# Kernel optimization log

Measured on AMD Instinct MI355X. Metric: run time of the kernel, lower is better.

The kernel has to match this reference:

```python
import jax, jax.numpy as jnp
import numpy as np

N_Q = 4; K = 4; IMG = 28; PAD = IMG + 2  # pad right/bottom so edge windows exist
N_WIN = 14 * 14  # stride-2 windows over 28x28


def _window_idx():
    # Faithful to torch: flatten the (possibly truncated) window row-major,
    # then pad with zeros AT THE END of the flattened vector.
    zero = PAD * PAD - 1  # padded image is zero there
    rows = []
    for i in range(0, IMG - 1, 2):
        for j in range(0, IMG - 1, 2):
            h = min(K, IMG - i); w = min(K, IMG - j)
            ids = [(i + r) * PAD + (j + c) for r in range(h) for c in range(w)]
            ids += [zero] * (K * K - len(ids))
            rows.append(ids)
    return np.asarray(rows, np.int32)  # [196, 16]

_WIDX = _window_idx()
# wire 0 is the most-significant bit of the 16-dim statevector index
_BITS = ((np.arange(16)[None, :] >> (3 - np.arange(4))[:, None]) & 1)
_ZSIGN = (1.0 - 2.0 * _BITS).astype(np.float32)  # [4, 16] PauliZ eigenvalues
# Four CRZ gates (control i, target (i+1)%4) are all diagonal -> combined diagonal phase
_CRZ_SIGNS = np.zeros(16, np.float32)
for _b in range(16):
    s = 0
    for _i in range(4):
        c = (_b >> (3 - _i)) & 1
        t = (_b >> (3 - ((_i + 1) % 4))) & 1
        s += c * (2 * t - 1)
    _CRZ_SIGNS[_b] = s
_H = (np.array([[1, 1], [1, -1]], np.complex64) / np.sqrt(2.0)).astype(np.complex64)


def _rz(a):  # a [B] -> [B,2,2]: diag(e^{-i a/2}, e^{+i a/2})
    em = jnp.exp(-0.5j * a); ep = jnp.exp(0.5j * a); z = jnp.zeros_like(em)
    return jnp.stack([jnp.stack([em, z], -1), jnp.stack([z, ep], -1)], -2)


def _ry(a):  # a [...] -> [...,2,2]
    c = jnp.cos(0.5 * a); s = jnp.sin(0.5 * a)
    return jnp.stack([jnp.stack([c, -s], -1), jnp.stack([s, c], -1)], -2).astype(jnp.complex64)


def _apply1q(state, U, w):  # state [B,16], U [B,2,2] or [2,2], wire w (0=MSB)
    L = 2 ** w; R = 2 ** (3 - w)
    s = state.reshape(-1, L, 2, R)
    if U.ndim == 2:
        out = jnp.einsum('ij,bajc->baic', U, s)
    else:
        out = jnp.einsum('bij,bajc->baic', U, s)
    return out.reshape(-1, 16)


def reference(x, crz_theta, ry_theta, fc1_w, fc1_b, fc2_w, fc2_b):
    B = x.shape[0]
    xp = jnp.pad(x[:, 0], ((0, 0), (0, 2), (0, 2))).reshape(B, -1)  # [B, 900]
    wins = xp[:, jnp.asarray(_WIDX)]              # [B, 196, 16]
    wins = jnp.transpose(wins, (1, 0, 2))         # [196, B, 16] for scan

    crz_diag = jnp.exp(0.5j * crz_theta * jnp.asarray(_CRZ_SIGNS))  # [16]
    Ry = _ry(ry_theta)                            # shared trainable RY, [2,2]
    H = jnp.asarray(_H)
    zsT = jnp.asarray(_ZSIGN).T                   # [16, 4]

    def step(state, f):  # state [B,16] complex64 persists ACROSS windows (no reset in source)
        for w in range(4):
            # compose H then the encoder rotations on this wire into one 2x2 per batch elem
            U = jnp.broadcast_to(H, (B, 2, 2))
            n = 5 if w < 3 else 1  # wire 3 only gets rz(f[15])
            for i in range(n):
                a = f[:, w * 5 + i]
                M = _rz(a) if i % 2 == 0 else _ry(a)  # gates = rz,ry,rz,ry,rz
                U = jnp.einsum('bij,bjk->bik', M, U)
            state = _apply1q(state, U, w)
        state = state * crz_diag[None, :]          # ring of CRZ gates (diagonal)
        for w in range(4):
            state = _apply1q(state, Ry, w)
        probs = state.real ** 2 + state.imag ** 2
        return state, probs @ zsT                  # [B, 4] PauliZ expectations

    state0 = jnp.zeros((B, 16), jnp.complex64).at[:, 0].set(1.0)
    _, outs = jax.lax.scan(step, state0, wins)     # [196, B, 4]
    feats = jnp.transpose(outs, (1, 0, 2)).reshape(B, N_WIN * 4)  # window-major concat
    h1 = feats @ fc1_w.T + fc1_b
    h1 = jnp.where(h1 > 0, h1, 0.1 * h1)           # LeakyReLU(0.1)
    return h1 @ fc2_w.T + fc2_b


def setup_inputs() -> dict:
    key = jax.random.key(0)
    ks = jax.random.split(key, 7)
    B = 16384
    return {
        'x': jax.random.normal(ks[0], (B, 1, 28, 28), jnp.float32),
        'crz_theta': jax.random.normal(ks[1], (), jnp.float32),
        'ry_theta': jax.random.normal(ks[2], (), jnp.float32),
        'fc1_w': jax.random.normal(ks[3], (20, 784), jnp.float32) * 0.03,
        'fc1_b': jnp.zeros((20,), jnp.float32),
        'fc2_w': jax.random.normal(ks[4], (2, 20), jnp.float32) * 0.1,
        'fc2_b': jnp.zeros((2,), jnp.float32),
    }
```

## Files before the change

kernel.cpp:

```cpp
#include <hip/hip_runtime.h>

#define RS2f 0.70710678118654752f

#define QP_XOR1 0xB1
#define QP_XOR2 0x4E
#define QP_BC0  0x00
#define QP_BC1  0x55
#define QP_BC2  0xAA
#define QP_BC3  0xFF

typedef float v2f __attribute__((ext_vector_type(2)));

template<int CTRL> __device__ __forceinline__ float dppf(float x) {
  return __int_as_float(__builtin_amdgcn_update_dpp(
      0, __float_as_int(x), CTRL, 0xF, 0xF, true));
}
template<int CTRL> __device__ __forceinline__ v2f dpp2(v2f v) {
  v2f r; r.x = dppf<CTRL>(v.x); r.y = dppf<CTRL>(v.y); return r;
}

__device__ __forceinline__ float sxor(float x, int sm) {
  return __int_as_float(__float_as_int(x) ^ sm);
}


__device__ __forceinline__ v2f pk_fma_rlo(v2f c, v2f x, v2f acc) {
  v2f d;
  asm("v_pk_fma_f32 %0, %1, %2, %3 op_sel:[0,0,0] op_sel_hi:[0,1,1]"
      : "=v"(d) : "v"(c), "v"(x), "v"(acc));
  return d;
}
__device__ __forceinline__ v2f pk_fma_nrlo(v2f c, v2f x, v2f acc) {
  v2f d;
  asm("v_pk_fma_f32 %0, %1, %2, %3 op_sel:[0,0,0] op_sel_hi:[0,1,1] neg_lo:[1,0,0] neg_hi:[1,0,0]"
      : "=v"(d) : "v"(c), "v"(x), "v"(acc));
  return d;
}
__device__ __forceinline__ v2f pk_fma_rhip(v2f c, v2f x, v2f acc) {
  v2f d;
  asm("v_pk_fma_f32 %0, %1, %2, %3 op_sel:[1,1,0] op_sel_hi:[1,0,1] neg_lo:[0,1,0]"
      : "=v"(d) : "v"(c), "v"(x), "v"(acc));
  return d;
}
__device__ __forceinline__ v2f pk_fma_rhic(v2f c, v2f x, v2f acc) {
  v2f d;
  asm("v_pk_fma_f32 %0, %1, %2, %3 op_sel:[1,1,0] op_sel_hi:[1,0,1] neg_hi:[0,1,0]"
      : "=v"(d) : "v"(c), "v"(x), "v"(acc));
  return d;
}
__device__ __forceinline__ v2f pk_mul_rhip(v2f c, v2f x) {
  v2f d;
  asm("v_pk_mul_f32 %0, %1, %2 op_sel:[1,1] op_sel_hi:[1,0] neg_lo:[0,1]"
      : "=v"(d) : "v"(c), "v"(x));
  return d;
}
__device__ __forceinline__ v2f pk_mul_rhi(v2f c, v2f x) {
  v2f d;
  asm("v_pk_mul_f32 %0, %1, %2 op_sel:[1,0] op_sel_hi:[1,1]"
      : "=v"(d) : "v"(c), "v"(x));
  return d;
}

__device__ __forceinline__ void hsc(float x, float* s, float* c) {
  float t = x * 0.07957747154594767f;
  *s = __builtin_amdgcn_sinf(t);
  *c = __builtin_amdgcn_cosf(t);
}

__device__ __forceinline__ void build_gate(float a0, float a1, float a2, float a3, float a4,
                                           v2f &WA, v2f &WB) {
  float sBp, cBp, sBm, cBm, sC, cC, sP, cP, sM, cM;
  hsc(a1 + a3, &sBp, &cBp);
  hsc(a1 - a3, &sBm, &cBm);
  hsc(a2,      &sC,  &cC);
  hsc(a0 + a4, &sP,  &cP);
  hsc(a0 - a4, &sM,  &cM);
  float m00r =  cBp * cC, m00i = -cBm * sC;
  float m01r = -sBp * cC, m01i =  sBm * sC;
  float alr = fmaf(m00r, cP,  m00i * sP);
  float ali = fmaf(m00i, cP, -m00r * sP);
  float ber = fmaf(m01r, cM, -m01i * sM);
  float bei = fmaf(m01i, cM,  m01r * sM);
  WA.x = RS2f * (alr + ber); WA.y = RS2f * (ali + bei);
  WB.x = RS2f * (alr - ber); WB.y = RS2f * (ali - bei);
}

#define PICK_FULL                                                            \
  a0 = l0 ? P[0][0] : l1 ? P[1][1] : l2 ? P[2][2] : P[3][3];                 \
  a1 = l0 ? P[0][1] : l1 ? P[1][2] : l2 ? P[2][3] : 0.f;                     \
  a2 = l0 ? P[0][2] : l1 ? P[1][3] : l2 ? P[3][0] : 0.f;                     \
  a3 = l0 ? P[0][3] : l1 ? P[2][0] : l2 ? P[3][1] : 0.f;                     \
  a4 = l0 ? P[1][0] : l1 ? P[2][1] : l2 ? P[3][2] : 0.f;

#define PICK_W2                                                              \
  a0 = l0 ? P[0][0] : l1 ? P[2][1] : 0.f;                                    \
  a1 = l0 ? P[0][1] : l1 ? P[3][0] : 0.f;                                    \
  a2 = l0 ? P[1][0] : l1 ? P[3][1] : 0.f;                                    \
  a3 = l0 ? P[1][1] : 0.f;                                                   \
  a4 = l0 ? P[2][0] : 0.f;

#define PICK_H2                                                              \
  a0 = l0 ? P[0][0] : l1 ? P[1][1] : 0.f;                                    \
  a1 = l0 ? P[0][1] : l1 ? P[1][2] : 0.f;                                    \
  a2 = l0 ? P[0][2] : l1 ? P[1][3] : 0.f;                                    \
  a3 = l0 ? P[0][3] : 0.f;                                                   \
  a4 = l0 ? P[1][0] : 0.f;

#define PICK_22                                                              \
  a0 = l0 ? P[0][0] : 0.f;                                                   \
  a1 = l0 ? P[0][1] : 0.f;                                                   \
  a2 = l0 ? P[1][0] : 0.f;                                                   \
  a3 = l0 ? P[1][1] : 0.f;                                                   \
  a4 = 0.f;

#define APPLY_Z do {                                                         \
  { v2f UA = dpp2<QP_BC0>(WcA), UB = dpp2<QP_BC0>(WcB);                      \
    UA.x = sxor(UA.x, sm0); UB.y = sxor(UB.y, sm0);                          \
    _Pragma("unroll")                                                        \
    for (int k = 0; k < 4; ++k) {                                            \
      v2f p = dpp2<QP_XOR2>(s[k]);                                           \
      v2f a = s[k];                                                          \
      s[k] = pk_fma_rlo(UA, a, pk_fma_rhip(UA, a,                            \
               pk_fma_rlo(UB, p, pk_mul_rhip(UB, p))));                      \
    } }                                                                      \
  { v2f UA = dpp2<QP_BC1>(WcA), UB = dpp2<QP_BC1>(WcB);                      \
    UA.x = sxor(UA.x, sm1); UB.y = sxor(UB.y, sm1);                          \
    _Pragma("unroll")                                                        \
    for (int k = 0; k < 4; ++k) {                                            \
      v2f p = dpp2<QP_XOR1>(s[k]);                                           \
      v2f a = s[k];                                                          \
      s[k] = pk_fma_rlo(UA, a, pk_fma_rhip(UA, a,                            \
               pk_fma_rlo(UB, p, pk_mul_rhip(UB, p))));                      \
    } }                                                                      \
  { v2f W0 = dpp2<QP_BC2>(WcA), W1 = dpp2<QP_BC2>(WcB);                      \
    _Pragma("unroll")                                                        \
    for (int k = 0; k < 2; ++k) {                                            \
      v2f lo = s[k], hi = s[k+2];                                            \
      s[k]   = pk_fma_rlo(W0, lo, pk_fma_rhip(W0, lo,                        \
                 pk_fma_rlo(W1, hi, pk_mul_rhip(W1, hi))));                  \
      s[k+2] = pk_fma_rlo(W1, lo, pk_fma_rhic(W1, lo,                        \
                 pk_fma_nrlo(W0, hi, pk_mul_rhip(W0, hi))));                 \
    } }                                                                      \
  { v2f W0 = dpp2<QP_BC3>(WcA), W1 = dpp2<QP_BC3>(WcB);                      \
    _Pragma("unroll")                                                        \
    for (int k = 0; k < 4; k += 2) {                                         \
      v2f lo = s[k], hi = s[k+1];                                            \
      s[k]   = pk_fma_rlo(W0, lo, pk_fma_rhip(W0, lo,                        \
                 pk_fma_rlo(W1, hi, pk_mul_rhip(W1, hi))));                  \
      s[k+1] = pk_fma_rlo(W1, lo, pk_fma_rhic(W1, lo,                        \
                 pk_fma_nrlo(W0, hi, pk_mul_rhip(W0, hi))));                 \
    } }                                                                      \
  _Pragma("unroll")                                                          \
  for (int k = 0; k < 4; ++k)                                                \
    s[k] = pk_fma_rlo(czv[k], s[k], pk_mul_rhip(czv[k], s[k]));              \
  _Pragma("unroll")                                                          \
  for (int k = 0; k < 4; ++k) {                                              \
    v2f p = dpp2<QP_XOR2>(s[k]);                                             \
    s[k] = pk_fma_rlo(RY0, s[k], pk_mul_rhi(RY0, p));                        \
  }                                                                          \
  _Pragma("unroll")                                                          \
  for (int k = 0; k < 4; ++k) {                                              \
    v2f p = dpp2<QP_XOR1>(s[k]);                                             \
    s[k] = pk_fma_rlo(RY1, s[k], pk_mul_rhi(RY1, p));                        \
  }                                                                          \
  _Pragma("unroll")                                                          \
  for (int k = 0; k < 2; ++k) {                                              \
    v2f lo = s[k], hi = s[k+2];                                              \
    s[k]   = pk_fma_rlo(RA_, lo, pk_mul_rhi(RA_, hi));                       \
    s[k+2] = pk_fma_rlo(RB_, lo, pk_mul_rhi(RB_, hi));                       \
  }                                                                          \
  _Pragma("unroll")                                                          \
  for (int k = 0; k < 4; k += 2) {                                           \
    v2f lo = s[k], hi = s[k+1];                                              \
    s[k]   = pk_fma_rlo(RA_, lo, pk_mul_rhi(RA_, hi));                       \
    s[k+1] = pk_fma_rlo(RB_, lo, pk_mul_rhi(RB_, hi));                       \
  }                                                                          \
  { v2f q0 = s[0]*s[0], q1 = s[1]*s[1], q2 = s[2]*s[2], q3 = s[3]*s[3];      \
    float p0 = q0.x + q0.y, p1 = q1.x + q1.y;                                \
    float p2 = q2.x + q2.y, p3 = q3.x + q3.y;                                \
    float s01 = p0 + p1, s23 = p2 + p3;                                      \
    float t_  = s01 + s23;                                                   \
    np0 = sxor(t_, sm0);                                                     \
    np1 = sxor(t_, sm1);                                                     \
    np2 = s01 - s23;                                                         \
    np3 = (p0 - p1) + (p2 - p3);                                             \
  }                                                                          \
} while (0)

#define BF_FOLD do {                                                         \
  float o0 = pd0, o1 = pd1, o2 = pd2, o3 = pd3;                              \
  o0 += dppf<QP_XOR1>(o0); o0 += dppf<QP_XOR2>(o0);                          \
  o1 += dppf<QP_XOR1>(o1); o1 += dppf<QP_XOR2>(o1);                          \
  o2 += dppf<QP_XOR1>(o2); o2 += dppf<QP_XOR2>(o2);                          \
  o3 += dppf<QP_XOR1>(o3); o3 += dppf<QP_XOR2>(o3);                          \
  const float* wp = swl + pdWin * 4;                                         \
  float4 wv0 = *(const float4*)(wp);                                         \
  float4 wv1 = *(const float4*)(wp + 784);                                   \
  float4 wv2 = *(const float4*)(wp + 1568);                                  \
  float4 wv3 = *(const float4*)(wp + 2352);                                  \
  float4 wv4 = *(const float4*)(wp + 3136);                                  \
  h1[0] = fmaf(wv0.x, o0, fmaf(wv0.y, o1, fmaf(wv0.z, o2, fmaf(wv0.w, o3, h1[0])))); \
  h1[1] = fmaf(wv1.x, o0, fmaf(wv1.y, o1, fmaf(wv1.z, o2, fmaf(wv1.w, o3, h1[1])))); \
  h1[2] = fmaf(wv2.x, o0, fmaf(wv2.y, o1, fmaf(wv2.z, o2, fmaf(wv2.w, o3, h1[2])))); \
  h1[3] = fmaf(wv3.x, o0, fmaf(wv3.y, o1, fmaf(wv3.z, o2, fmaf(wv3.w, o3, h1[3])))); \
  h1[4] = fmaf(wv4.x, o0, fmaf(wv4.y, o1, fmaf(wv4.z, o2, fmaf(wv4.w, o3, h1[4])))); \
} while (0)

#define SHIFT_PEND(WIN)  pd0 = np0; pd1 = np1; pd2 = np2; pd3 = np3; pdWin = (WIN);
#define ROTATE_W  WcA = WnA; WcB = WnB;

__global__ void __launch_bounds__(256)
quanv_kernel(const float* __restrict__ x,
             const float* __restrict__ crz_t,
             const float* __restrict__ ry_t,
             const float* __restrict__ fc1_w,
             const float* __restrict__ fc1_b,
             const float* __restrict__ fc2_w,
             const float* __restrict__ fc2_b,
             float* __restrict__ out, int B)
{
  __shared__ float sw[20 * 784];
  const int tid = threadIdx.x;
  for (int i = tid; i < (20 * 784) / 4; i += 256)
    ((float4*)sw)[i] = ((const float4*)fc1_w)[i];
  __syncthreads();

  const int l = tid & 3;
  const int b = (blockIdx.x * 256 + tid) >> 2;
  if (b >= B) return;
  const float* img = x + (size_t)b * 784;
  const bool l0 = (l == 0), l1 = (l == 1), l2 = (l == 2);

  const float theta = crz_t[0];
  const float ryt   = ry_t[0];
  float cry, sry;
  hsc(ryt, &sry, &cry);
  const float sgn0 = (l & 2) ? sry : -sry;
  const float sgn1 = (l & 1) ? sry : -sry;
  const int sm0 = (l & 2) ? (int)0x80000000 : 0;
  const int sm1 = (l & 1) ? (int)0x80000000 : 0;

  v2f RY0, RY1, RA_, RB_;
  RY0.x = cry; RY0.y = sgn0;
  RY1.x = cry; RY1.y = sgn1;
  RA_.x = cry; RA_.y = -sry;
  RB_.x = sry; RB_.y = cry;

  float g0,g1,g2,g3;
  if      (l == 0) { g0= 0.f; g1=-1.f; g2=-1.f; g3=0.f; }
  else if (l == 1) { g0=-1.f; g1=-2.f; g2= 0.f; g3=1.f; }
  else if (l == 2) { g0=-1.f; g1= 0.f; g2=-2.f; g3=1.f; }
  else             { g0= 0.f; g1= 1.f; g2= 1.f; g3=4.f; }
  v2f czv[4];
  { float sz, cz;
    hsc(theta*g0, &sz, &cz); czv[0].x = cz; czv[0].y = sz;
    hsc(theta*g1, &sz, &cz); czv[1].x = cz; czv[1].y = sz;
    hsc(theta*g2, &sz, &cz); czv[2].x = cz; czv[2].y = sz;
    hsc(theta*g3, &sz, &cz); czv[3].x = cz; czv[3].y = sz; }

  v2f s[4];
#pragma unroll
  for (int k = 0; k < 4; ++k) { s[k].x = 0.f; s[k].y = 0.f; }
  if (l == 0) s[0].x = 1.f;

  float h1[5];
#pragma unroll
  for (int j = 0; j < 5; ++j) h1[j] = 0.f;
  const float* swl = sw + 5 * l * 784;

  float P[4][4];
  float a0, a1, a2, a3, a4;
  v2f WcA, WcB, WnA, WnB;
  float np0, np1, np2, np3;
  float pd0 = 0.f, pd1 = 0.f, pd2 = 0.f, pd3 = 0.f;
  int pdWin = 0;

#pragma unroll 1
  for (int wi = 0; wi < 13; ++wi) {
    const float* imgw = img + (2 * wi) * 28;

#pragma unroll
    for (int r = 0; r < 4; ++r) {
      float4 v = *(const float4*)(imgw + r * 28);
      P[r][0]=v.x; P[r][1]=v.y; P[r][2]=v.z; P[r][3]=v.w;
    }
    PICK_FULL;
    build_gate(a0, a1, a2, a3, a4, WcA, WcB);

    float2 Q0 = *(const float2*)(imgw + 0 * 28 + 4);
    float2 Q1 = *(const float2*)(imgw + 1 * 28 + 4);
    float2 Q2 = *(const float2*)(imgw + 2 * 28 + 4);
    float2 Q3 = *(const float2*)(imgw + 3 * 28 + 4);

#pragma unroll 2
    for (int wj = 1; wj <= 12; ++wj) {
      P[0][0]=P[0][2]; P[0][1]=P[0][3]; P[0][2]=Q0.x; P[0][3]=Q0.y;
      P[1][0]=P[1][2]; P[1][1]=P[1][3]; P[1][2]=Q1.x; P[1][3]=Q1.y;
      P[2][0]=P[2][2]; P[2][1]=P[2][3]; P[2][2]=Q2.x; P[2][3]=Q2.y;
      P[3][0]=P[3][2]; P[3][1]=P[3][3]; P[3][2]=Q3.x; P[3][3]=Q3.y;
      const int c0n = (wj < 12) ? (2 * wj + 4) : 24;
      Q0 = *(const float2*)(imgw + 0 * 28 + c0n);
      Q1 = *(const float2*)(imgw + 1 * 28 + c0n);
      Q2 = *(const float2*)(imgw + 2 * 28 + c0n);
      Q3 = *(const float2*)(imgw + 3 * 28 + c0n);
      PICK_FULL;
      build_gate(a0, a1, a2, a3, a4, WnA, WnB);
      APPLY_Z;
      BF_FOLD;
      SHIFT_PEND(wi * 14 + wj - 1);
      ROTATE_W;
    }

#pragma unroll
    for (int r = 0; r < 4; ++r) {
      P[r][0] = P[r][2]; P[r][1] = P[r][3]; P[r][2] = 0.f; P[r][3] = 0.f;
    }
    PICK_W2;
    build_gate(a0, a1, a2, a3, a4, WnA, WnB);
    APPLY_Z;
    BF_FOLD;
    SHIFT_PEND(wi * 14 + 12);
    ROTATE_W;
    APPLY_Z;
    BF_FOLD;
    SHIFT_PEND(wi * 14 + 13);
  }

  {
    const float* imgw = img + 26 * 28;
#pragma unroll
    for (int r = 0; r < 2; ++r) {
      float4 v = *(const float4*)(imgw + r * 28);
      P[r][0]=v.x; P[r][1]=v.y; P[r][2]=v.z; P[r][3]=v.w;
    }
#pragma unroll
    for (int r = 2; r < 4; ++r) { P[r][0]=0.f; P[r][1]=0.f; P[r][2]=0.f; P[r][3]=0.f; }
    PICK_H2;
    build_gate(a0, a1, a2, a3, a4, WcA, WcB);

    float2 Q0 = *(const float2*)(imgw + 4);
    float2 Q1 = *(const float2*)(imgw + 28 + 4);

#pragma unroll 2
    for (int wj = 1; wj <= 12; ++wj) {
      P[0][0]=P[0][2]; P[0][1]=P[0][3]; P[0][2]=Q0.x; P[0][3]=Q0.y;
      P[1][0]=P[1][2]; P[1][1]=P[1][3]; P[1][2]=Q1.x; P[1][3]=Q1.y;
      const int c0n = (wj < 12) ? (2 * wj + 4) : 24;
      Q0 = *(const float2*)(imgw + c0n);
      Q1 = *(const float2*)(imgw + 28 + c0n);
      PICK_H2;
      build_gate(a0, a1, a2, a3, a4, WnA, WnB);
      APPLY_Z;
      BF_FOLD;
      SHIFT_PEND(182 + wj - 1);
      ROTATE_W;
    }

    P[0][0]=P[0][2]; P[0][1]=P[0][3]; P[0][2]=0.f; P[0][3]=0.f;
    P[1][0]=P[1][2]; P[1][1]=P[1][3]; P[1][2]=0.f; P[1][3]=0.f;
    PICK_22;
    build_gate(a0, a1, a2, a3, a4, WnA, WnB);
    APPLY_Z;
    BF_FOLD;
    SHIFT_PEND(182 + 12);
    ROTATE_W;
    APPLY_Z;
    BF_FOLD;
    SHIFT_PEND(182 + 13);
  }

  BF_FOLD;

  float pa = 0.f, pb = 0.f;
#pragma unroll
  for (int j = 0; j < 5; ++j) {
    const int r = 5 * l + j;
    float v = h1[j] + fc1_b[r];
    v = (v > 0.f) ? v : 0.1f * v;
    pa = fmaf(fc2_w[r],      v, pa);
    pb = fmaf(fc2_w[20 + r], v, pb);
  }
  pa += dppf<QP_XOR1>(pa); pa += dppf<QP_XOR2>(pa);
  pb += dppf<QP_XOR1>(pb); pb += dppf<QP_XOR2>(pb);
  if (l == 0) {
    float2 res; res.x = pa + fc2_b[0]; res.y = pb + fc2_b[1];
    *(float2*)(out + (size_t)b * 2) = res;
  }
}

extern "C" void kernel_launch(void* const* d_in, const int* in_sizes, int n_in,
                              void* d_out, int out_size, void* d_ws, size_t ws_size,
                              hipStream_t stream) {
  const float* x      = (const float*)d_in[0];
  const float* crz_t  = (const float*)d_in[1];
  const float* ry_t   = (const float*)d_in[2];
  const float* fc1_w  = (const float*)d_in[3];
  const float* fc1_b  = (const float*)d_in[4];
  const float* fc2_w  = (const float*)d_in[5];
  const float* fc2_b  = (const float*)d_in[6];
  float* out = (float*)d_out;
  const int B = in_sizes[0] / 784;
  const int grid = (B * 4 + 255) / 256;
  quanv_kernel<<<grid, 256, 0, stream>>>(x, crz_t, ry_t, fc1_w, fc1_b,
                                         fc2_w, fc2_b, out, B);
}
```

Baseline: 205.5 us.

## Load only per-lane window pixels and pack fc1 accumulation into packed FMAs

```diff
diff --git a/kernel.cpp b/kernel.cpp
--- a/kernel.cpp
+++ b/kernel.cpp
@@ -10,6 +10,8 @@
 #define QP_BC3  0xFF
 
 typedef float v2f __attribute__((ext_vector_type(2)));
+typedef float v4f __attribute__((ext_vector_type(4)));
+typedef v4f v4fu __attribute__((aligned(4)));
 
 template<int CTRL> __device__ __forceinline__ float dppf(float x) {
   return __int_as_float(__builtin_amdgcn_update_dpp(
@@ -22,6 +24,9 @@
 __device__ __forceinline__ float sxor(float x, int sm) {
   return __int_as_float(__float_as_int(x) ^ sm);
 }
+__device__ __forceinline__ v2f vlo(v4f v) { return __builtin_shufflevector(v, v, 0, 1); }
+__device__ __forceinline__ v2f vhi(v4f v) { return __builtin_shufflevector(v, v, 2, 3); }
+__device__ __forceinline__ v4f loadu4(const float* p) { return *(const v4fu*)p; }
 
 
 __device__ __forceinline__ v2f pk_fma_rlo(v2f c, v2f x, v2f acc) {
@@ -85,33 +90,19 @@
   WB.x = RS2f * (alr - ber); WB.y = RS2f * (ali - bei);
 }
 
-#define PICK_FULL                                                            \
-  a0 = l0 ? P[0][0] : l1 ? P[1][1] : l2 ? P[2][2] : P[3][3];                 \
-  a1 = l0 ? P[0][1] : l1 ? P[1][2] : l2 ? P[2][3] : 0.f;                     \
-  a2 = l0 ? P[0][2] : l1 ? P[1][3] : l2 ? P[3][0] : 0.f;                     \
-  a3 = l0 ? P[0][3] : l1 ? P[2][0] : l2 ? P[3][1] : 0.f;                     \
-  a4 = l0 ? P[1][0] : l1 ? P[2][1] : l2 ? P[3][2] : 0.f;
-
-#define PICK_W2                                                              \
-  a0 = l0 ? P[0][0] : l1 ? P[2][1] : 0.f;                                    \
-  a1 = l0 ? P[0][1] : l1 ? P[3][0] : 0.f;                                    \
-  a2 = l0 ? P[1][0] : l1 ? P[3][1] : 0.f;                                    \
-  a3 = l0 ? P[1][1] : 0.f;                                                   \
-  a4 = l0 ? P[2][0] : 0.f;
-
-#define PICK_H2                                                              \
-  a0 = l0 ? P[0][0] : l1 ? P[1][1] : 0.f;                                    \
-  a1 = l0 ? P[0][1] : l1 ? P[1][2] : 0.f;                                    \
-  a2 = l0 ? P[0][2] : l1 ? P[1][3] : 0.f;                                    \
-  a3 = l0 ? P[0][3] : 0.f;                                                   \
-  a4 = l0 ? P[1][0] : 0.f;
-
-#define PICK_22                                                              \
-  a0 = l0 ? P[0][0] : 0.f;                                                   \
-  a1 = l0 ? P[0][1] : 0.f;                                                   \
-  a2 = l0 ? P[1][0] : 0.f;                                                   \
-  a3 = l0 ? P[1][1] : 0.f;                                                   \
-  a4 = 0.f;
+#define SEL_MAIN                                                             \
+  a0 = l3 ? Ac.w : Ac.x;                                                     \
+  a1 = l3 ? 0.f  : Ac.y;                                                     \
+  a2 = l2 ? Bc.x : (l3 ? 0.f : Ac.z);                                        \
+  a3 = l0 ? Ac.w : (l1 ? Bc.x : (l2 ? Bc.y : 0.f));                          \
+  a4 = l0 ? Bc.x : (l1 ? Bc.y : (l2 ? Bc.z : 0.f));
+
+#define SEL_TAIL                                                             \
+  a0 = l0 ? Ac.x : (l1 ? Ac.y : 0.f);                                        \
+  a1 = l0 ? Ac.y : (l1 ? Ac.z : 0.f);                                        \
+  a2 = l0 ? Ac.z : (l1 ? Ac.w : 0.f);                                        \
+  a3 = l0 ? Ac.w : 0.f;                                                      \
+  a4 = l0 ? Bc.x : 0.f;
 
 #define APPLY_Z do {                                                         \
   { v2f UA = dpp2<QP_BC0>(WcA), UB = dpp2<QP_BC0>(WcB);                      \
@@ -180,33 +171,40 @@
     float p2 = q2.x + q2.y, p3 = q3.x + q3.y;                                \
     float s01 = p0 + p1, s23 = p2 + p3;                                      \
     float t_  = s01 + s23;                                                   \
-    np0 = sxor(t_, sm0);                                                     \
-    np1 = sxor(t_, sm1);                                                     \
-    np2 = s01 - s23;                                                         \
-    np3 = (p0 - p1) + (p2 - p3);                                             \
+    npA.x = sxor(t_, sm0);                                                   \
+    npA.y = sxor(t_, sm1);                                                   \
+    npB.x = s01 - s23;                                                       \
+    npB.y = (p0 - p1) + (p2 - p3);                                           \
   }                                                                          \
 } while (0)
 
-#define BF_FOLD do {                                                         \
-  float o0 = pd0, o1 = pd1, o2 = pd2, o3 = pd3;                              \
-  o0 += dppf<QP_XOR1>(o0); o0 += dppf<QP_XOR2>(o0);                          \
-  o1 += dppf<QP_XOR1>(o1); o1 += dppf<QP_XOR2>(o1);                          \
-  o2 += dppf<QP_XOR1>(o2); o2 += dppf<QP_XOR2>(o2);                          \
-  o3 += dppf<QP_XOR1>(o3); o3 += dppf<QP_XOR2>(o3);                          \
+#define BF_LOAD                                                              \
   const float* wp = swl + pdWin * 4;                                         \
-  float4 wv0 = *(const float4*)(wp);                                         \
-  float4 wv1 = *(const float4*)(wp + 784);                                   \
-  float4 wv2 = *(const float4*)(wp + 1568);                                  \
-  float4 wv3 = *(const float4*)(wp + 2352);                                  \
-  float4 wv4 = *(const float4*)(wp + 3136);                                  \
-  h1[0] = fmaf(wv0.x, o0, fmaf(wv0.y, o1, fmaf(wv0.z, o2, fmaf(wv0.w, o3, h1[0])))); \
-  h1[1] = fmaf(wv1.x, o0, fmaf(wv1.y, o1, fmaf(wv1.z, o2, fmaf(wv1.w, o3, h1[1])))); \
-  h1[2] = fmaf(wv2.x, o0, fmaf(wv2.y, o1, fmaf(wv2.z, o2, fmaf(wv2.w, o3, h1[2])))); \
-  h1[3] = fmaf(wv3.x, o0, fmaf(wv3.y, o1, fmaf(wv3.z, o2, fmaf(wv3.w, o3, h1[3])))); \
-  h1[4] = fmaf(wv4.x, o0, fmaf(wv4.y, o1, fmaf(wv4.z, o2, fmaf(wv4.w, o3, h1[4])))); \
+  v4f wv0 = *(const v4f*)(wp);                                               \
+  v4f wv1 = *(const v4f*)(wp + 784);                                         \
+  v4f wv2 = *(const v4f*)(wp + 1568);                                        \
+  v4f wv3 = *(const v4f*)(wp + 2352);                                        \
+  v4f wv4 = *(const v4f*)(wp + 3136);
+
+#define BF_USE do {                                                          \
+  v2f oA = pdA, oB = pdB;                                                    \
+  oA = oA + dpp2<QP_XOR1>(oA); oA = oA + dpp2<QP_XOR2>(oA);                  \
+  oB = oB + dpp2<QP_XOR1>(oB); oB = oB + dpp2<QP_XOR2>(oB);                  \
+  h1v[0] = __builtin_elementwise_fma(vlo(wv0), oA,                           \
+             __builtin_elementwise_fma(vhi(wv0), oB, h1v[0]));               \
+  h1v[1] = __builtin_elementwise_fma(vlo(wv1), oA,                           \
+             __builtin_elementwise_fma(vhi(wv1), oB, h1v[1]));               \
+  h1v[2] = __builtin_elementwise_fma(vlo(wv2), oA,                           \
+             __builtin_elementwise_fma(vhi(wv2), oB, h1v[2]));               \
+  h1v[3] = __builtin_elementwise_fma(vlo(wv3), oA,                           \
+             __builtin_elementwise_fma(vhi(wv3), oB, h1v[3]));               \
+  h1v[4] = __builtin_elementwise_fma(vlo(wv4), oA,                           \
+             __builtin_elementwise_fma(vhi(wv4), oB, h1v[4]));               \
 } while (0)
 
-#define SHIFT_PEND(WIN)  pd0 = np0; pd1 = np1; pd2 = np2; pd3 = np3; pdWin = (WIN);
+#define BF_FOLD do { BF_LOAD; BF_USE; } while (0)
+
+#define SHIFT_PEND(WIN)  pdA = npA; pdB = npB; pdWin = (WIN);
 #define ROTATE_W  WcA = WnA; WcB = WnB;
 
 __global__ void __launch_bounds__(256)
@@ -229,7 +227,10 @@
   const int b = (blockIdx.x * 256 + tid) >> 2;
   if (b >= B) return;
   const float* img = x + (size_t)b * 784;
-  const bool l0 = (l == 0), l1 = (l == 1), l2 = (l == 2);
+  const bool l0 = (l == 0), l1 = (l == 1), l2 = (l == 2), l3 = (l == 3);
+
+  const int offA = l3 ? 84 : l * 29;
+  const int offB = (l >= 2) ? 84 : (l + 1) * 28;
 
   const float theta = crz_t[0];
   const float ryt   = ry_t[0];
@@ -261,62 +262,62 @@
   v2f s[4];
 #pragma unroll
   for (int k = 0; k < 4; ++k) { s[k].x = 0.f; s[k].y = 0.f; }
-  if (l == 0) s[0].x = 1.f;
-
-  float h1[5];
+  if (l0) s[0].x = 1.f;
+
+  v2f h1v[5];
 #pragma unroll
-  for (int j = 0; j < 5; ++j) h1[j] = 0.f;
+  for (int j = 0; j < 5; ++j) { h1v[j].x = 0.f; h1v[j].y = 0.f; }
   const float* swl = sw + 5 * l * 784;
 
-  float P[4][4];
   float a0, a1, a2, a3, a4;
   v2f WcA, WcB, WnA, WnB;
-  float np0, np1, np2, np3;
-  float pd0 = 0.f, pd1 = 0.f, pd2 = 0.f, pd3 = 0.f;
+  v2f npA, npB;
+  v2f pdA, pdB;
+  pdA.x = 0.f; pdA.y = 0.f; pdB.x = 0.f; pdB.y = 0.f;
   int pdWin = 0;
 
 #pragma unroll 1
   for (int wi = 0; wi < 13; ++wi) {
-    const float* imgw = img + (2 * wi) * 28;
-
-#pragma unroll
-    for (int r = 0; r < 4; ++r) {
-      float4 v = *(const float4*)(imgw + r * 28);
-      P[r][0]=v.x; P[r][1]=v.y; P[r][2]=v.z; P[r][3]=v.w;
-    }
-    PICK_FULL;
-    build_gate(a0, a1, a2, a3, a4, WcA, WcB);
-
-    float2 Q0 = *(const float2*)(imgw + 0 * 28 + 4);
-    float2 Q1 = *(const float2*)(imgw + 1 * 28 + 4);
-    float2 Q2 = *(const float2*)(imgw + 2 * 28 + 4);
-    float2 Q3 = *(const float2*)(imgw + 3 * 28 + 4);
+    const float* rp = img + (2 * wi) * 28;
+    const float* pA = rp + offA;
+    const float* pB = rp + offB;
+
+    {
+      v4f Ac = loadu4(pA);
+      v4f Bc = loadu4(pB);
+      SEL_MAIN;
+      build_gate(a0, a1, a2, a3, a4, WcA, WcB);
+    }
+
+    v4f An = loadu4(pA + 2);
+    v4f Bn = loadu4(pB + 2);
 
 #pragma unroll 2
     for (int wj = 1; wj <= 12; ++wj) {
-      P[0][0]=P[0][2]; P[0][1]=P[0][3]; P[0][2]=Q0.x; P[0][3]=Q0.y;
-      P[1][0]=P[1][2]; P[1][1]=P[1][3]; P[1][2]=Q1.x; P[1][3]=Q1.y;
-      P[2][0]=P[2][2]; P[2][1]=P[2][3]; P[2][2]=Q2.x; P[2][3]=Q2.y;
-      P[3][0]=P[3][2]; P[3][1]=P[3][3]; P[3][2]=Q3.x; P[3][3]=Q3.y;
-      const int c0n = (wj < 12) ? (2 * wj + 4) : 24;
-      Q0 = *(const float2*)(imgw + 0 * 28 + c0n);
-      Q1 = *(const float2*)(imgw + 1 * 28 + c0n);
-      Q2 = *(const float2*)(imgw + 2 * 28 + c0n);
-      Q3 = *(const float2*)(imgw + 3 * 28 + c0n);
-      PICK_FULL;
+      BF_LOAD;
+      v4f Ac = An, Bc = Bn;
+      const int jn = (wj < 12) ? 2 * (wj + 1) : 24;
+      An = loadu4(pA + jn);
+      Bn = loadu4(pB + jn);
+      SEL_MAIN;
       build_gate(a0, a1, a2, a3, a4, WnA, WnB);
       APPLY_Z;
-      BF_FOLD;
+      BF_USE;
       SHIFT_PEND(wi * 14 + wj - 1);
       ROTATE_W;
     }
 
-#pragma unroll
-    for (int r = 0; r < 4; ++r) {
-      P[r][0] = P[r][2]; P[r][1] = P[r][3]; P[r][2] = 0.f; P[r][3] = 0.f;
-    }
-    PICK_W2;
-    build_gate(a0, a1, a2, a3, a4, WnA, WnB);
+    {
+      v2f C0 = *(const v2f*)(rp + (l1 ? 56 : 0)  + 26);
+      v2f C1 = *(const v2f*)(rp + (l1 ? 84 : 28) + 26);
+      v2f C2 = *(const v2f*)(rp + (l1 ? 84 : 56) + 26);
+      a0 = l0 ? C0.x : (l1 ? C0.y : 0.f);
+      a1 = l0 ? C0.y : (l1 ? C1.x : 0.f);
+      a2 = l0 ? C1.x : (l1 ? C1.y : 0.f);
+      a3 = l0 ? C1.y : 0.f;
+      a4 = l0 ? C2.x : 0.f;
+      build_gate(a0, a1, a2, a3, a4, WnA, WnB);
+    }
     APPLY_Z;
     BF_FOLD;
     SHIFT_PEND(wi * 14 + 12);
@@ -327,39 +328,44 @@
   }
 
   {
-    const float* imgw = img + 26 * 28;
-#pragma unroll
-    for (int r = 0; r < 2; ++r) {
-      float4 v = *(const float4*)(imgw + r * 28);
-      P[r][0]=v.x; P[r][1]=v.y; P[r][2]=v.z; P[r][3]=v.w;
-    }
-#pragma unroll
-    for (int r = 2; r < 4; ++r) { P[r][0]=0.f; P[r][1]=0.f; P[r][2]=0.f; P[r][3]=0.f; }
-    PICK_H2;
-    build_gate(a0, a1, a2, a3, a4, WcA, WcB);
-
-    float2 Q0 = *(const float2*)(imgw + 4);
-    float2 Q1 = *(const float2*)(imgw + 28 + 4);
+    const float* pA = img + 728 + (l1 ? 28 : 0);
+    const float* pB = img + 756;
+
+    {
+      v4f Ac = loadu4(pA);
+      v4f Bc = loadu4(pB);
+      SEL_TAIL;
+      build_gate(a0, a1, a2, a3, a4, WcA, WcB);
+    }
+
+    v4f An = loadu4(pA + 2);
+    v4f Bn = loadu4(pB + 2);
 
 #pragma unroll 2
     for (int wj = 1; wj <= 12; ++wj) {
-      P[0][0]=P[0][2]; P[0][1]=P[0][3]; P[0][2]=Q0.x; P[0][3]=Q0.y;
-      P[1][0]=P[1][2]; P[1][1]=P[1][3]; P[1][2]=Q1.x; P[1][3]=Q1.y;
-      const int c0n = (wj < 12) ? (2 * wj + 4) : 24;
-      Q0 = *(const float2*)(imgw + c0n);
-      Q1 = *(const float2*)(imgw + 28 + c0n);
-      PICK_H2;
+      BF_LOAD;
+      v4f Ac = An, Bc = Bn;
+      const int jn = (wj < 12) ? 2 * (wj + 1) : 24;
+      An = loadu4(pA + jn);
+      Bn = loadu4(pB + jn);
+      SEL_TAIL;
       build_gate(a0, a1, a2, a3, a4, WnA, WnB);
       APPLY_Z;
-      BF_FOLD;
+      BF_USE;
       SHIFT_PEND(182 + wj - 1);
       ROTATE_W;
     }
 
-    P[0][0]=P[0][2]; P[0][1]=P[0][3]; P[0][2]=0.f; P[0][3]=0.f;
-    P[1][0]=P[1][2]; P[1][1]=P[1][3]; P[1][2]=0.f; P[1][3]=0.f;
-    PICK_22;
-    build_gate(a0, a1, a2, a3, a4, WnA, WnB);
+    {
+      v2f D0 = *(const v2f*)(img + 26 * 28 + 26);
+      v2f D1 = *(const v2f*)(img + 27 * 28 + 26);
+      a0 = l0 ? D0.x : 0.f;
+      a1 = l0 ? D0.y : 0.f;
+      a2 = l0 ? D1.x : 0.f;
+      a3 = l0 ? D1.y : 0.f;
+      a4 = 0.f;
+      build_gate(a0, a1, a2, a3, a4, WnA, WnB);
+    }
     APPLY_Z;
     BF_FOLD;
     SHIFT_PEND(182 + 12);
@@ -375,14 +381,14 @@
 #pragma unroll
   for (int j = 0; j < 5; ++j) {
     const int r = 5 * l + j;
-    float v = h1[j] + fc1_b[r];
+    float v = h1v[j].x + h1v[j].y + fc1_b[r];
     v = (v > 0.f) ? v : 0.1f * v;
     pa = fmaf(fc2_w[r],      v, pa);
     pb = fmaf(fc2_w[20 + r], v, pb);
   }
   pa += dppf<QP_XOR1>(pa); pa += dppf<QP_XOR2>(pa);
   pb += dppf<QP_XOR1>(pb); pb += dppf<QP_XOR2>(pb);
-  if (l == 0) {
+  if (l0) {
     float2 res; res.x = pa + fc2_b[0]; res.y = pb + fc2_b[1];
     *(float2*)(out + (size_t)b * 2) = res;
   }
```

Measured after the change: 214.0 us. +4.1%, slower.
